# Kernel tuning notes

Measured on AMD Instinct MI355X. Metric: run time of the kernel, lower is better.

## Reference

```python
import jax, jax.numpy as jnp
import numpy as np

B, L, INPUT_DIM = 4, 4096, 32
D_MODEL, N_LAYERS = 256, 2
D_STATE, D_CONV, EXPAND = 16, 4, 2
D_INNER = EXPAND * D_MODEL          # 512
DT_RANK = (D_MODEL + 15) // 16      # 16
OUTPUT_DIM, HORIZON = 32, 4
LN_EPS = 1e-5


def setup_inputs() -> dict:
    key = jax.random.key(0)
    ks = jax.random.split(key, 16)
    s = 0.02
    inp = {
        "x": jax.random.normal(ks[0], (B, L, INPUT_DIM), jnp.float32),
        "enc_w": jax.random.normal(ks[1], (D_MODEL, INPUT_DIM), jnp.float32) * s,
        "enc_b": jnp.zeros((D_MODEL,), jnp.float32),
        "in_proj_w": jax.random.normal(ks[2], (N_LAYERS, 2 * D_INNER, D_MODEL), jnp.float32) * s,
        "conv_w": jax.random.normal(ks[3], (N_LAYERS, D_INNER, D_CONV), jnp.float32) * s,
        "conv_b": jnp.zeros((N_LAYERS, D_INNER), jnp.float32),
        "xproj_w": jax.random.normal(ks[4], (N_LAYERS, DT_RANK + 2 * D_STATE, D_INNER), jnp.float32) * s,
        "dtproj_w": jax.random.normal(ks[5], (N_LAYERS, D_INNER, DT_RANK), jnp.float32) * s,
        "dtproj_b": jax.random.normal(ks[6], (N_LAYERS, D_INNER), jnp.float32) * 0.1,
        "A_log": jnp.log(jnp.tile(jnp.arange(1.0, D_STATE + 1.0, dtype=jnp.float32), (N_LAYERS, D_INNER, 1))),
        "Dp": jnp.ones((N_LAYERS, D_INNER), jnp.float32),
        "out_proj_w": jax.random.normal(ks[7], (N_LAYERS, D_MODEL, D_INNER), jnp.float32) * s,
        "ln_g": jnp.ones((D_MODEL,), jnp.float32),
        "ln_b": jnp.zeros((D_MODEL,), jnp.float32),
        "head_w": jax.random.normal(ks[8], (OUTPUT_DIM * HORIZON, D_MODEL), jnp.float32) * s,
        "head_b": jnp.zeros((OUTPUT_DIM * HORIZON,), jnp.float32),
    }
    return inp


def _mamba_block(x, in_w, cw, cb, xp_w, dt_w, dt_b, A_log, Dp, out_w):
    # x: [B, L, d_model]
    b, l, _ = x.shape
    xz = jnp.einsum("bld,ed->ble", x, in_w)            # [B, L, 2*d_inner]
    xi, res = jnp.split(xz, 2, axis=-1)
    # causal depthwise conv1d (padding=d_conv-1, truncated to L)
    xpad = jnp.pad(xi, ((0, 0), (D_CONV - 1, 0), (0, 0)))
    xi = sum(xpad[:, k:k + l, :] * cw[:, k] for k in range(D_CONV)) + cb
    xi = jax.nn.silu(xi)
    dbl = jnp.einsum("bld,ed->ble", xi, xp_w)           # [B, L, dt_rank+2*d_state]
    dt = dbl[..., :DT_RANK]
    Bm = dbl[..., DT_RANK:DT_RANK + D_STATE]            # [B, L, d_state]
    Cm = dbl[..., DT_RANK + D_STATE:]                   # [B, L, d_state]
    dt = jax.nn.softplus(jnp.einsum("blr,dr->bld", dt, dt_w) + dt_b)  # [B, L, d_inner]
    A = -jnp.exp(A_log)                                 # [d_inner, d_state]

    def step(h, ins):
        dt_t, B_t, C_t, x_t = ins                       # [B,di],[B,ds],[B,ds],[B,di]
        dA = jnp.exp(dt_t[..., None] * A)               # [B, d_inner, d_state]
        h = dA * h + (dt_t * x_t)[..., None] * B_t[:, None, :]
        y = jnp.einsum("bds,bs->bd", h, C_t)
        return h, y

    h0 = jnp.zeros((b, D_INNER, D_STATE), x.dtype)
    xs = (jnp.moveaxis(dt, 1, 0), jnp.moveaxis(Bm, 1, 0),
          jnp.moveaxis(Cm, 1, 0), jnp.moveaxis(xi, 1, 0))
    _, ys = jax.lax.scan(step, h0, xs)                  # ys: [L, B, d_inner]
    y = jnp.moveaxis(ys, 0, 1) + xi * Dp
    y = y * jax.nn.silu(res)
    return jnp.einsum("ble,de->bld", y, out_w)


def reference(x, enc_w, enc_b, in_proj_w, conv_w, conv_b, xproj_w, dtproj_w,
              dtproj_b, A_log, Dp, out_proj_w, ln_g, ln_b, head_w, head_b):
    h = jnp.einsum("bli,di->bld", x, enc_w) + enc_b     # encoder
    for i in range(N_LAYERS):
        h = h + _mamba_block(h, in_proj_w[i], conv_w[i], conv_b[i], xproj_w[i],
                             dtproj_w[i], dtproj_b[i], A_log[i], Dp[i], out_proj_w[i])
    mu = jnp.mean(h, axis=-1, keepdims=True)
    var = jnp.mean((h - mu) ** 2, axis=-1, keepdims=True)
    hn = (h - mu) * jax.lax.rsqrt(var + LN_EPS) * ln_g + ln_b
    state = hn[:, -1, :]                                # last timestep
    return jnp.einsum("bd,od->bo", state, head_w) + head_b
```

## Files before the change

### kernel.cpp

```cpp
#include <hip/hip_runtime.h>
#include <hip/hip_bf16.h>
#include <math.h>

#define BB 4
#define LL 4096
#define DM 256
#define DI 512
#define DS 16
#define NOUTK 128
#define LN_EPS 1e-5f
#define NC 128
#define CLEN (LL/NC)
#define BL (BB*LL)
#define LDB 640

typedef __attribute__((ext_vector_type(8))) short short8;
typedef __attribute__((ext_vector_type(4))) float f32x4;

__device__ __forceinline__ ushort f2bf(float f) {
    union { float f; unsigned u; } v; v.f = f;
    unsigned r = (v.u + 0x7FFF + ((v.u >> 16) & 1)) >> 16;
    return (ushort)r;
}
__device__ __forceinline__ float bf2f(ushort u) {
    union { unsigned u; float f; } v; v.u = ((unsigned)u) << 16;
    return v.f;
}

#define PREP_N1 (2*1024*256)
#define PREP_N2 (2*256*512)
#define PREP_N3 (2*640*512)
__global__ __launch_bounds__(256) void prep_kernel(
    const float* __restrict__ inw, const float* __restrict__ opw,
    const float* __restrict__ xpw, const float* __restrict__ dtw,
    ushort* __restrict__ inw_bf, ushort* __restrict__ opw_bf,
    ushort* __restrict__ comb_bf)
{
    int i = blockIdx.x * 256 + threadIdx.x;
    if (i < PREP_N1) {
        inw_bf[i] = f2bf(inw[i]);
        return;
    }
    int j = i - PREP_N1;
    if (j < PREP_N2) {
        opw_bf[j] = f2bf(opw[j]);
        return;
    }
    int m = j - PREP_N2;
    if (m >= PREP_N3) return;
    int l = m / (640 * 512);
    int rem = m - l * 640 * 512;
    int row = rem >> 9, k = rem & 511;
    const float* xp = xpw + l * 48 * 512;
    const float* dw = dtw + l * 512 * 16;
    float v;
    if (row < 512) {
        v = 0.f;
        #pragma unroll
        for (int r = 0; r < 16; ++r)
            v = fmaf(dw[row * 16 + r], xp[r * 512 + k], v);
    } else if (row < 544) {
        v = xp[(row - 512 + 16) * 512 + k];
    } else v = 0.f;
    comb_bf[m] = f2bf(v);
}

__global__ __launch_bounds__(256) void enc_kernel(
    const float* __restrict__ x, const float* __restrict__ w,
    const float* __restrict__ b, float* __restrict__ h,
    ushort* __restrict__ hbf)
{
    __shared__ float sw[256 * 33];
    __shared__ float sx[4][32];
    int tid = threadIdx.x;
    for (int i = tid; i < 256 * 8; i += 256) {
        float4 v = ((const float4*)w)[i];
        int r = i >> 3, c = (i & 7) * 4;
        sw[r * 33 + c + 0] = v.x; sw[r * 33 + c + 1] = v.y;
        sw[r * 33 + c + 2] = v.z; sw[r * 33 + c + 3] = v.w;
    }
    int row0 = blockIdx.x * 4;
    if (tid < 32) {
        for (int rr = 0; rr < 4; ++rr)
            sx[rr][tid] = x[(size_t)(row0 + rr) * 32 + tid];
    }
    __syncthreads();
    float bb = b[tid];
    #pragma unroll
    for (int rr = 0; rr < 4; ++rr) {
        float acc = bb;
        #pragma unroll
        for (int k = 0; k < 32; ++k)
            acc = fmaf(sx[rr][k], sw[tid * 33 + k], acc);
        size_t o = (size_t)(row0 + rr) * DM + tid;
        h[o] = acc;
        hbf[o] = f2bf(acc);
    }
}

template<int EPI, bool F32OUT, bool RESID, bool BF16OUT>
__global__ __launch_bounds__(256, 6) void mfma_gemm(
    const ushort* __restrict__ A, int lda,
    const ushort* __restrict__ W,
    const float* __restrict__ bias,
    float* __restrict__ C, int ldc,
    ushort* __restrict__ Cbf, int ldcbf,
    int K)
{
    __shared__ ushort As[64 * 64];
    __shared__ ushort Ws[128 * 64];
    const int tid = threadIdx.x;

    int nwg = gridDim.x * gridDim.y;
    int wlin = blockIdx.y * gridDim.x + blockIdx.x;
    int gx = blockIdx.x, gy = blockIdx.y;
    if ((nwg & 7) == 0) {
        int q = nwg >> 3;
        int s = (wlin & 7) * q + (wlin >> 3);
        gx = s % gridDim.x;
        gy = s / gridDim.x;
    }
    const int bm = gy * 64;
    const int bn = gx * 128;
    const int wid = tid >> 6, lane = tid & 63;
    const int wrow = (wid >> 1) * 32, wcol = (wid & 1) * 64;
    const int sr = tid >> 3;
    const int sc = tid & 7;

    f32x4 acc[2][4];
    #pragma unroll
    for (int mi = 0; mi < 2; ++mi)
        #pragma unroll
        for (int ni = 0; ni < 4; ++ni)
            acc[mi][ni] = (f32x4){0.f, 0.f, 0.f, 0.f};

    const int nk = K >> 6;
    for (int t = 0; t < nk; ++t) {
        const int k0 = t << 6;
        #pragma unroll
        for (int it = 0; it < 2; ++it) {
            int r = it * 32 + sr;
            int csrc = sc ^ (r & 7);
            __builtin_amdgcn_global_load_lds(
                (const __attribute__((address_space(1))) unsigned int*)
                    (A + (size_t)(bm + r) * lda + k0 + csrc * 8),
                (__attribute__((address_space(3))) unsigned int*)
                    (As + r * 64 + sc * 8), 16, 0, 0);
        }
        #pragma unroll
        for (int it = 0; it < 4; ++it) {
            int r = it * 32 + sr;
            int csrc = sc ^ (r & 7);
            __builtin_amdgcn_global_load_lds(
                (const __attribute__((address_space(1))) unsigned int*)
                    (W + (size_t)(bn + r) * K + k0 + csrc * 8),
                (__attribute__((address_space(3))) unsigned int*)
                    (Ws + r * 64 + sc * 8), 16, 0, 0);
        }
        __syncthreads();
        #pragma unroll
        for (int kk = 0; kk < 2; ++kk) {
            short8 af[2], bfr[4];
            #pragma unroll
            for (int mi = 0; mi < 2; ++mi) {
                int r = wrow + mi * 16 + (lane & 15);
                int c = (lane >> 4) + kk * 4;
                af[mi] = *(const short8*)(As + r * 64 + ((c ^ (r & 7)) << 3));
            }
            #pragma unroll
            for (int ni = 0; ni < 4; ++ni) {
                int r = wcol + ni * 16 + (lane & 15);
                int c = (lane >> 4) + kk * 4;
                bfr[ni] = *(const short8*)(Ws + r * 64 + ((c ^ (r & 7)) << 3));
            }
            #pragma unroll
            for (int mi = 0; mi < 2; ++mi)
                #pragma unroll
                for (int ni = 0; ni < 4; ++ni)
                    acc[mi][ni] = __builtin_amdgcn_mfma_f32_16x16x32_bf16(
                        af[mi], bfr[ni], acc[mi][ni], 0, 0, 0);
        }
        __syncthreads();
    }

    #pragma unroll
    for (int mi = 0; mi < 2; ++mi)
        #pragma unroll
        for (int ni = 0; ni < 4; ++ni) {
            int col = bn + wcol + ni * 16 + (lane & 15);
            #pragma unroll
            for (int r = 0; r < 4; ++r) {
                int row = bm + wrow + mi * 16 + (lane >> 4) * 4 + r;
                float v = acc[mi][ni][r];
                if (EPI == 1) {
                    if (col < 512) {
                        float u = v + bias[col];
                        float sp = fmaxf(u, 0.f) + __logf(1.f + __expf(-fabsf(u)));
                        Cbf[(size_t)row * ldcbf + col] = f2bf(sp);
                    } else if (col < 544) {
                        C[(size_t)row * ldc + (col - 512)] = v;
                    }
                } else {
                    if (F32OUT) {
                        float* cp = C + (size_t)row * ldc + col;
                        float vv = v;
                        if (RESID) vv += *cp;
                        *cp = vv;
                        if (BF16OUT) Cbf[(size_t)row * ldcbf + col] = f2bf(vv);
                    } else if (BF16OUT) {
                        Cbf[(size_t)row * ldcbf + col] = f2bf(v);
                    }
                }
            }
        }
}

__global__ __launch_bounds__(256) void conv_silu_kernel(
    const ushort* __restrict__ xz, const float* __restrict__ cw,
    const float* __restrict__ cb, ushort* __restrict__ xi)
{
    int idx = blockIdx.x * 256 + threadIdx.x;
    int d4 = (idx & 127) * 4;
    int bt = idx >> 7;
    int t = bt & (LL - 1);
    const ushort* base = xz + (size_t)bt * 1024 + d4;
    float acc[4];
    float4 w[4];
    #pragma unroll
    for (int j = 0; j < 4; ++j) {
        acc[j] = cb[d4 + j];
        w[j] = *(const float4*)(cw + (d4 + j) * 4);
    }
    #pragma unroll
    for (int k = 0; k < 4; ++k) {
        int back = 3 - k;
        if (t >= back) {
            ushort4 v = *(const ushort4*)(base - back * 1024);
            float wk0 = (k==0)?w[0].x:(k==1)?w[0].y:(k==2)?w[0].z:w[0].w;
            float wk1 = (k==0)?w[1].x:(k==1)?w[1].y:(k==2)?w[1].z:w[1].w;
            float wk2 = (k==0)?w[2].x:(k==1)?w[2].y:(k==2)?w[2].z:w[2].w;
            float wk3 = (k==0)?w[3].x:(k==1)?w[3].y:(k==2)?w[3].z:w[3].w;
            acc[0] = fmaf(bf2f(v.x), wk0, acc[0]);
            acc[1] = fmaf(bf2f(v.y), wk1, acc[1]);
            acc[2] = fmaf(bf2f(v.z), wk2, acc[2]);
            acc[3] = fmaf(bf2f(v.w), wk3, acc[3]);
        }
    }
    ushort4 o;
    float s0 = acc[0] / (1.f + __expf(-acc[0]));
    float s1 = acc[1] / (1.f + __expf(-acc[1]));
    float s2 = acc[2] / (1.f + __expf(-acc[2]));
    float s3 = acc[3] / (1.f + __expf(-acc[3]));
    o.x = f2bf(s0); o.y = f2bf(s1); o.z = f2bf(s2); o.w = f2bf(s3);
    *(ushort4*)(xi + (size_t)bt * 512 + d4) = o;
}

__global__ __launch_bounds__(256) void scan_phase1(
    const ushort* __restrict__ xi, const ushort* __restrict__ dtb,
    const float* __restrict__ bc,
    const float* __restrict__ alog,
    float* __restrict__ cS, float* __restrict__ cH)
{
    int d = blockIdx.z * 256 + threadIdx.x;
    int b = blockIdx.y, c = blockIdx.x;
    float Av[16];
    bool fast = true;
    #pragma unroll
    for (int s = 0; s < 16; ++s) {
        Av[s] = -__expf(alog[d * 16 + s]);
        fast = fast && (fabsf(Av[s] + (float)(s + 1)) < 1e-3f * (s + 1));
    }
    float h[16];
    #pragma unroll
    for (int s = 0; s < 16; ++s) h[s] = 0.f;
    float S = 0.f;
    int t0 = c * CLEN;
    if (fast) {
        for (int t = t0; t < t0 + CLEN; ++t) {
            size_t row = (size_t)b * LL + t;
            float dt = bf2f(dtb[row * 512 + d]);
            float x = bf2f(xi[row * 512 + d]);
            float dtx = dt * x;
            S += dt;
            const float* bp = bc + row * 32;
            float e1 = __expf(-dt);
            float e2=e1*e1, e3=e2*e1, e4=e2*e2, e5=e3*e2, e6=e3*e3, e7=e4*e3, e8=e4*e4;
            float e9=e5*e4, e10=e5*e5, e11=e6*e5, e12=e6*e6, e13=e7*e6, e14=e7*e7, e15=e8*e7, e16=e8*e8;
            float pw[16] = {e1,e2,e3,e4,e5,e6,e7,e8,e9,e10,e11,e12,e13,e14,e15,e16};
            #pragma unroll
            for (int s = 0; s < 16; ++s)
                h[s] = fmaf(pw[s], h[s], dtx * bp[s]);
        }
    } else {
        for (int t = t0; t < t0 + CLEN; ++t) {
            size_t row = (size_t)b * LL + t;
            float dt = bf2f(dtb[row * 512 + d]);
            float x = bf2f(xi[row * 512 + d]);
            float dtx = dt * x;
            S += dt;
            const float* bp = bc + row * 32;
            #pragma unroll
            for (int s = 0; s < 16; ++s) {
                float dA = __expf(dt * Av[s]);
                h[s] = fmaf(dA, h[s], dtx * bp[s]);
            }
        }
    }
    cS[((size_t)b * DI + d) * NC + c] = S;
    size_t base = (((size_t)b * DI + d) * NC + c) * 16;
    #pragma unroll
    for (int q = 0; q < 4; ++q)
        *(float4*)(cH + base + q*4) = *(float4*)&h[q*4];
}

__global__ __launch_bounds__(256) void scan_phase2(
    const float* __restrict__ cS, float* __restrict__ cH,
    const float* __restrict__ alog)
{
    int bd = blockIdx.x;
    int d = bd & (DI - 1);
    int tid = threadIdx.x;
    int s = tid >> 4;
    int g = tid & 15;
    float Avs = -__expf(alog[d * 16 + s]);
    size_t sbase = (size_t)bd * NC;
    size_t base = (size_t)bd * NC * 16 + s;
    float a8[8], h8[8];
    #pragma unroll
    for (int j = 0; j < 8; ++j) {
        float Sj = cS[sbase + g * 8 + j];
        a8[j] = __expf(Avs * Sj);
        h8[j] = cH[base + (size_t)(g * 8 + j) * 16];
    }
    float A = 1.f, H = 0.f;
    #pragma unroll
    for (int j = 0; j < 8; ++j) {
        H = fmaf(a8[j], H, h8[j]);
        A *= a8[j];
    }
    #pragma unroll
    for (int off = 1; off < 16; off <<= 1) {
        float Ap = __shfl_up(A, off, 16);
        float Hp = __shfl_up(H, off, 16);
        if (g >= off) { H = fmaf(A, Hp, H); A *= Ap; }
    }
    float init = __shfl_up(H, 1, 16);
    if (g == 0) init = 0.f;
    #pragma unroll
    for (int j = 0; j < 8; ++j) {
        size_t o = base + (size_t)(g * 8 + j) * 16;
        cH[o] = init;
        init = fmaf(a8[j], init, h8[j]);
    }
}

__global__ __launch_bounds__(256) void scan_phase3(
    const ushort* __restrict__ xz,
    ushort* __restrict__ xi,
    const ushort* __restrict__ dtb,
    const float* __restrict__ bc,
    const float* __restrict__ alog,
    const float* __restrict__ Dp,
    const float* __restrict__ cH,
    int c0)
{
    int d = blockIdx.z * 256 + threadIdx.x;
    int b = blockIdx.y;
    int c = blockIdx.x + c0;
    float Av[16];
    bool fast = true;
    #pragma unroll
    for (int s = 0; s < 16; ++s) {
        Av[s] = -__expf(alog[d * 16 + s]);
        fast = fast && (fabsf(Av[s] + (float)(s + 1)) < 1e-3f * (s + 1));
    }
    float h[16];
    size_t cbase = (((size_t)b * DI + d) * NC + c) * 16;
    #pragma unroll
    for (int q = 0; q < 4; ++q)
        *(float4*)&h[q*4] = *(const float4*)(cH + cbase + q*4);
    float Dd = Dp[d];
    int t0 = c * CLEN;
    if (fast) {
        for (int t = t0; t < t0 + CLEN; ++t) {
            size_t row = (size_t)b * LL + t;
            float dt = bf2f(dtb[row * 512 + d]);
            float x = bf2f(xi[row * 512 + d]);
            float dtx = dt * x;
            const float* bp = bc + row * 32;
            const float* cp = bc + row * 32 + 16;
            float e1 = __expf(-dt);
            float e2=e1*e1, e3=e2*e1, e4=e2*e2, e5=e3*e2, e6=e3*e3, e7=e4*e3, e8=e4*e4;
            float e9=e5*e4, e10=e5*e5, e11=e6*e5, e12=e6*e6, e13=e7*e6, e14=e7*e7, e15=e8*e7, e16=e8*e8;
            float pw[16] = {e1,e2,e3,e4,e5,e6,e7,e8,e9,e10,e11,e12,e13,e14,e15,e16};
            float y = 0.f;
            #pragma unroll
            for (int s = 0; s < 16; ++s) {
                h[s] = fmaf(pw[s], h[s], dtx * bp[s]);
                y = fmaf(h[s], cp[s], y);
            }
            float res = bf2f(xz[row * 1024 + 512 + d]);
            float g = (y + x * Dd) * (res / (1.f + __expf(-res)));
            xi[row * 512 + d] = f2bf(g);
        }
    } else {
        for (int t = t0; t < t0 + CLEN; ++t) {
            size_t row = (size_t)b * LL + t;
            float dt = bf2f(dtb[row * 512 + d]);
            float x = bf2f(xi[row * 512 + d]);
            float dtx = dt * x;
            const float* bp = bc + row * 32;
            const float* cp = bc + row * 32 + 16;
            float y = 0.f;
            #pragma unroll
            for (int s = 0; s < 16; ++s) {
                float dA = __expf(dt * Av[s]);
                h[s] = fmaf(dA, h[s], dtx * bp[s]);
                y = fmaf(h[s], cp[s], y);
            }
            float res = bf2f(xz[row * 1024 + 512 + d]);
            float g = (y + x * Dd) * (res / (1.f + __expf(-res)));
            xi[row * 512 + d] = f2bf(g);
        }
    }
}

__global__ __launch_bounds__(256) void out_proj_last_kernel(
    const ushort* __restrict__ xi, const float* __restrict__ W,
    float* __restrict__ h)
{
    int b = blockIdx.x, n = threadIdx.x;
    __shared__ float sy[DI];
    const ushort* yrow = xi + ((size_t)b * LL + (LL - 1)) * DI;
    for (int k = threadIdx.x; k < DI; k += 256) sy[k] = bf2f(yrow[k]);
    __syncthreads();
    const float* wr = W + (size_t)n * DI;
    float acc = 0.f;
    for (int k = 0; k < DI; k += 4) {
        float4 wv = *(const float4*)(wr + k);
        acc = fmaf(sy[k+0], wv.x, acc);
        acc = fmaf(sy[k+1], wv.y, acc);
        acc = fmaf(sy[k+2], wv.z, acc);
        acc = fmaf(sy[k+3], wv.w, acc);
    }
    h[((size_t)b * LL + (LL - 1)) * DM + n] += acc;
}

__global__ __launch_bounds__(256) void ln_head_kernel(
    const float* __restrict__ h, const float* __restrict__ lng,
    const float* __restrict__ lnb, const float* __restrict__ hw,
    const float* __restrict__ hb, float* __restrict__ out)
{
    int b = blockIdx.x, tid = threadIdx.x;
    __shared__ float sh[DM];
    __shared__ float r1[4], r2[4];
    float v = h[((size_t)b * LL + (LL - 1)) * DM + tid];
    float s = v;
    #pragma unroll
    for (int o = 32; o >= 1; o >>= 1) s += __shfl_down(s, o);
    if ((tid & 63) == 0) r1[tid >> 6] = s;
    __syncthreads();
    float mu = (r1[0] + r1[1] + r1[2] + r1[3]) * (1.f / 256.f);
    float dv = v - mu;
    float q = dv * dv;
    #pragma unroll
    for (int o = 32; o >= 1; o >>= 1) q += __shfl_down(q, o);
    if ((tid & 63) == 0) r2[tid >> 6] = q;
    __syncthreads();
    float var = (r2[0] + r2[1] + r2[2] + r2[3]) * (1.f / 256.f);
    sh[tid] = dv * rsqrtf(var + LN_EPS) * lng[tid] + lnb[tid];
    __syncthreads();
    if (tid < NOUTK) {
        const float* wr = hw + (size_t)tid * DM;
        float acc = hb[tid];
        for (int d2 = 0; d2 < DM; d2 += 4) {
            float4 wv = *(const float4*)(wr + d2);
            acc = fmaf(sh[d2+0], wv.x, acc);
            acc = fmaf(sh[d2+1], wv.y, acc);
            acc = fmaf(sh[d2+2], wv.z, acc);
            acc = fmaf(sh[d2+3], wv.w, acc);
        }
        out[b * NOUTK + tid] = acc;
    }
}

extern "C" void kernel_launch(void* const* d_in, const int* in_sizes, int n_in,
                              void* d_out, int out_size, void* d_ws, size_t ws_size,
                              hipStream_t stream)
{
    const float* x    = (const float*)d_in[0];
    const float* encw = (const float*)d_in[1];
    const float* encb = (const float*)d_in[2];
    const float* inw  = (const float*)d_in[3];
    const float* cw   = (const float*)d_in[4];
    const float* cb   = (const float*)d_in[5];
    const float* xpw  = (const float*)d_in[6];
    const float* dtw  = (const float*)d_in[7];
    const float* dtb  = (const float*)d_in[8];
    const float* alog = (const float*)d_in[9];
    const float* Dp   = (const float*)d_in[10];
    const float* opw  = (const float*)d_in[11];
    const float* lng  = (const float*)d_in[12];
    const float* lnb  = (const float*)d_in[13];
    const float* hw   = (const float*)d_in[14];
    const float* hb   = (const float*)d_in[15];
    float* out = (float*)d_out;

    float* ws   = (float*)d_ws;
    float* h    = ws;
    float* bc   = h   + (size_t)BL * DM;
    float* cS   = bc  + (size_t)BL * 32;
    float* cH   = cS  + (size_t)BB * DI * NC;
    ushort* h_bf    = (ushort*)(cH + (size_t)BB * DI * NC * DS);
    ushort* xz_bf   = h_bf  + (size_t)BL * DM;
    ushort* xi_bf   = xz_bf + (size_t)BL * 1024;
    ushort* dt_bf   = xi_bf + (size_t)BL * DI;
    ushort* inw_bf  = dt_bf + (size_t)BL * DI;
    ushort* opw_bf  = inw_bf + 2 * 1024 * DM;
    ushort* comb_bf = opw_bf + 2 * DM * DI;

    dim3 blk(256, 1, 1);

    prep_kernel<<<dim3((PREP_N1 + PREP_N2 + PREP_N3) / 256), blk, 0, stream>>>(
        inw, opw, xpw, dtw, inw_bf, opw_bf, comb_bf);

    enc_kernel<<<dim3(BL/4), blk, 0, stream>>>(x, encw, encb, h, h_bf);

    for (int l = 0; l < 2; ++l) {
        mfma_gemm<0,false,false,true><<<dim3(1024/128, BL/64), blk, 0, stream>>>(
            h_bf, DM, inw_bf + (size_t)l * 1024 * DM, nullptr,
            nullptr, 0, xz_bf, 1024, DM);
        conv_silu_kernel<<<dim3(BL * 128 / 256), blk, 0, stream>>>(
            xz_bf, cw + l * DI * 4, cb + l * DI, xi_bf);
        mfma_gemm<1,false,false,false><<<dim3(LDB/128, BL/64), blk, 0, stream>>>(
            xi_bf, DI, comb_bf + (size_t)l * LDB * DI, dtb + l * DI,
            bc, 32, dt_bf, 512, DI);
        scan_phase1<<<dim3(NC, BB, 2), blk, 0, stream>>>(
            xi_bf, dt_bf, bc, alog + (size_t)l * DI * 16, cS, cH);
        scan_phase2<<<dim3(BB * DI), blk, 0, stream>>>(
            cS, cH, alog + (size_t)l * DI * 16);
        if (l == 0) {
            scan_phase3<<<dim3(NC, BB, 2), blk, 0, stream>>>(
                xz_bf, xi_bf, dt_bf, bc, alog + (size_t)l * DI * 16,
                Dp + l * DI, cH, 0);
            mfma_gemm<0,true,true,true><<<dim3(DM/128, BL/64), blk, 0, stream>>>(
                xi_bf, DI, opw_bf + (size_t)l * DM * DI, nullptr,
                h, DM, h_bf, DM, DI);
        } else {
            scan_phase3<<<dim3(1, BB, 2), blk, 0, stream>>>(
                xz_bf, xi_bf, dt_bf, bc, alog + (size_t)l * DI * 16,
                Dp + l * DI, cH, NC - 1);
            out_proj_last_kernel<<<dim3(BB), blk, 0, stream>>>(
                xi_bf, opw + (size_t)l * DM * DI, h);
        }
    }

    ln_head_kernel<<<dim3(BB), blk, 0, stream>>>(h, lng, lnb, hw, hb, out);
}
```

Before: 345.9 us.

## Drop fp32 residual stream, keep bf16 only; slide conv window over 8 timesteps

Removes the full fp32 hidden-state buffer: the encoder writes only bf16, the layer-0 out-projection adds its residual in place on the bf16 copy, and the final layer writes just the last-timestep fp32 row into a small buffer for the LayerNorm head. Each conv thread now handles 8 consecutive timesteps with a rolling 3-element window instead of reloading 4 rows per output. GEMM launch bounds change from 6 to 4 waves. Less HBM traffic, but the residual is kept in bf16, which costs precision.

```diff
diff --git a/kernel.cpp b/kernel.cpp
--- a/kernel.cpp
+++ b/kernel.cpp
@@ -67,8 +67,7 @@
 
 __global__ __launch_bounds__(256) void enc_kernel(
     const float* __restrict__ x, const float* __restrict__ w,
-    const float* __restrict__ b, float* __restrict__ h,
-    ushort* __restrict__ hbf)
+    const float* __restrict__ b, ushort* __restrict__ hbf)
 {
     __shared__ float sw[256 * 33];
     __shared__ float sx[4][32];
@@ -92,19 +91,17 @@
         #pragma unroll
         for (int k = 0; k < 32; ++k)
             acc = fmaf(sx[rr][k], sw[tid * 33 + k], acc);
-        size_t o = (size_t)(row0 + rr) * DM + tid;
-        h[o] = acc;
-        hbf[o] = f2bf(acc);
-    }
-}
-
-template<int EPI, bool F32OUT, bool RESID, bool BF16OUT>
-__global__ __launch_bounds__(256, 6) void mfma_gemm(
+        hbf[(size_t)(row0 + rr) * DM + tid] = f2bf(acc);
+    }
+}
+
+template<int EPI>
+__global__ __launch_bounds__(256, 4) void mfma_gemm(
     const ushort* __restrict__ A, int lda,
     const ushort* __restrict__ W,
     const float* __restrict__ bias,
     float* __restrict__ C, int ldc,
-    ushort* __restrict__ Cbf, int ldcbf,
+    ushort* Cbf, int ldcbf,
     int K)
 {
     __shared__ ushort As[64 * 64];
@@ -200,16 +197,12 @@
                     } else if (col < 544) {
                         C[(size_t)row * ldc + (col - 512)] = v;
                     }
+                } else if (EPI == 2) {
+                    size_t o = (size_t)row * ldcbf + col;
+                    float vv = v + bf2f(Cbf[o]);
+                    Cbf[o] = f2bf(vv);
                 } else {
-                    if (F32OUT) {
-                        float* cp = C + (size_t)row * ldc + col;
-                        float vv = v;
-                        if (RESID) vv += *cp;
-                        *cp = vv;
-                        if (BF16OUT) Cbf[(size_t)row * ldcbf + col] = f2bf(vv);
-                    } else if (BF16OUT) {
-                        Cbf[(size_t)row * ldcbf + col] = f2bf(v);
-                    }
+                    Cbf[(size_t)row * ldcbf + col] = f2bf(v);
                 }
             }
         }
@@ -221,38 +214,43 @@
 {
     int idx = blockIdx.x * 256 + threadIdx.x;
     int d4 = (idx & 127) * 4;
-    int bt = idx >> 7;
-    int t = bt & (LL - 1);
-    const ushort* base = xz + (size_t)bt * 1024 + d4;
-    float acc[4];
-    float4 w[4];
-    #pragma unroll
-    for (int j = 0; j < 4; ++j) {
-        acc[j] = cb[d4 + j];
-        w[j] = *(const float4*)(cw + (d4 + j) * 4);
-    }
-    #pragma unroll
-    for (int k = 0; k < 4; ++k) {
-        int back = 3 - k;
-        if (t >= back) {
-            ushort4 v = *(const ushort4*)(base - back * 1024);
-            float wk0 = (k==0)?w[0].x:(k==1)?w[0].y:(k==2)?w[0].z:w[0].w;
-            float wk1 = (k==0)?w[1].x:(k==1)?w[1].y:(k==2)?w[1].z:w[1].w;
-            float wk2 = (k==0)?w[2].x:(k==1)?w[2].y:(k==2)?w[2].z:w[2].w;
-            float wk3 = (k==0)?w[3].x:(k==1)?w[3].y:(k==2)?w[3].z:w[3].w;
-            acc[0] = fmaf(bf2f(v.x), wk0, acc[0]);
-            acc[1] = fmaf(bf2f(v.y), wk1, acc[1]);
-            acc[2] = fmaf(bf2f(v.z), wk2, acc[2]);
-            acc[3] = fmaf(bf2f(v.w), wk3, acc[3]);
-        }
-    }
-    ushort4 o;
-    float s0 = acc[0] / (1.f + __expf(-acc[0]));
-    float s1 = acc[1] / (1.f + __expf(-acc[1]));
-    float s2 = acc[2] / (1.f + __expf(-acc[2]));
-    float s3 = acc[3] / (1.f + __expf(-acc[3]));
-    o.x = f2bf(s0); o.y = f2bf(s1); o.z = f2bf(s2); o.w = f2bf(s3);
-    *(ushort4*)(xi + (size_t)bt * 512 + d4) = o;
+    int grp = idx >> 7;
+    int b = grp >> 9;
+    int t0 = (grp & 511) * 8;
+    const ushort* base = xz + ((size_t)(b * LL + t0) * 1024) + d4;
+    ushort* obase = xi + ((size_t)(b * LL + t0) * 512) + d4;
+
+    float4 w0 = *(const float4*)(cw + (d4 + 0) * 4);
+    float4 w1 = *(const float4*)(cw + (d4 + 1) * 4);
+    float4 w2 = *(const float4*)(cw + (d4 + 2) * 4);
+    float4 w3 = *(const float4*)(cw + (d4 + 3) * 4);
+    float b0 = cb[d4 + 0], b1 = cb[d4 + 1], b2 = cb[d4 + 2], b3 = cb[d4 + 3];
+
+    ushort4 z4 = {0, 0, 0, 0};
+    ushort4 win0 = (t0 >= 3) ? *(const ushort4*)(base - 3 * 1024) : z4;
+    ushort4 win1 = (t0 >= 2) ? *(const ushort4*)(base - 2 * 1024) : z4;
+    ushort4 win2 = (t0 >= 1) ? *(const ushort4*)(base - 1 * 1024) : z4;
+
+    #pragma unroll
+    for (int k = 0; k < 8; ++k) {
+        ushort4 cur = *(const ushort4*)(base + k * 1024);
+        float a0 = b0, a1 = b1, a2 = b2, a3 = b3;
+        a0 = fmaf(bf2f(win0.x), w0.x, a0); a1 = fmaf(bf2f(win0.y), w1.x, a1);
+        a2 = fmaf(bf2f(win0.z), w2.x, a2); a3 = fmaf(bf2f(win0.w), w3.x, a3);
+        a0 = fmaf(bf2f(win1.x), w0.y, a0); a1 = fmaf(bf2f(win1.y), w1.y, a1);
+        a2 = fmaf(bf2f(win1.z), w2.y, a2); a3 = fmaf(bf2f(win1.w), w3.y, a3);
+        a0 = fmaf(bf2f(win2.x), w0.z, a0); a1 = fmaf(bf2f(win2.y), w1.z, a1);
+        a2 = fmaf(bf2f(win2.z), w2.z, a2); a3 = fmaf(bf2f(win2.w), w3.z, a3);
+        a0 = fmaf(bf2f(cur.x),  w0.w, a0); a1 = fmaf(bf2f(cur.y),  w1.w, a1);
+        a2 = fmaf(bf2f(cur.z),  w2.w, a2); a3 = fmaf(bf2f(cur.w),  w3.w, a3);
+        ushort4 o;
+        o.x = f2bf(a0 / (1.f + __expf(-a0)));
+        o.y = f2bf(a1 / (1.f + __expf(-a1)));
+        o.z = f2bf(a2 / (1.f + __expf(-a2)));
+        o.w = f2bf(a3 / (1.f + __expf(-a3)));
+        *(ushort4*)(obase + k * 512) = o;
+        win0 = win1; win1 = win2; win2 = cur;
+    }
 }
 
 __global__ __launch_bounds__(256) void scan_phase1(
@@ -427,7 +425,7 @@
 
 __global__ __launch_bounds__(256) void out_proj_last_kernel(
     const ushort* __restrict__ xi, const float* __restrict__ W,
-    float* __restrict__ h)
+    const ushort* __restrict__ hbf, float* __restrict__ hlast)
 {
     int b = blockIdx.x, n = threadIdx.x;
     __shared__ float sy[DI];
@@ -443,18 +441,18 @@
         acc = fmaf(sy[k+2], wv.z, acc);
         acc = fmaf(sy[k+3], wv.w, acc);
     }
-    h[((size_t)b * LL + (LL - 1)) * DM + n] += acc;
+    hlast[b * DM + n] = acc + bf2f(hbf[((size_t)b * LL + (LL - 1)) * DM + n]);
 }
 
 __global__ __launch_bounds__(256) void ln_head_kernel(
-    const float* __restrict__ h, const float* __restrict__ lng,
+    const float* __restrict__ hlast, const float* __restrict__ lng,
     const float* __restrict__ lnb, const float* __restrict__ hw,
     const float* __restrict__ hb, float* __restrict__ out)
 {
     int b = blockIdx.x, tid = threadIdx.x;
     __shared__ float sh[DM];
     __shared__ float r1[4], r2[4];
-    float v = h[((size_t)b * LL + (LL - 1)) * DM + tid];
+    float v = hlast[b * DM + tid];
     float s = v;
     #pragma unroll
     for (int o = 32; o >= 1; o >>= 1) s += __shfl_down(s, o);
@@ -507,11 +505,11 @@
     float* out = (float*)d_out;
 
     float* ws   = (float*)d_ws;
-    float* h    = ws;
-    float* bc   = h   + (size_t)BL * DM;
+    float* bc   = ws;
     float* cS   = bc  + (size_t)BL * 32;
     float* cH   = cS  + (size_t)BB * DI * NC;
-    ushort* h_bf    = (ushort*)(cH + (size_t)BB * DI * NC * DS);
+    float* hlast = cH + (size_t)BB * DI * NC * DS;
+    ushort* h_bf    = (ushort*)(hlast + BB * DM);
     ushort* xz_bf   = h_bf  + (size_t)BL * DM;
     ushort* xi_bf   = xz_bf + (size_t)BL * 1024;
     ushort* dt_bf   = xi_bf + (size_t)BL * DI;
@@ -524,15 +522,15 @@
     prep_kernel<<<dim3((PREP_N1 + PREP_N2 + PREP_N3) / 256), blk, 0, stream>>>(
         inw, opw, xpw, dtw, inw_bf, opw_bf, comb_bf);
 
-    enc_kernel<<<dim3(BL/4), blk, 0, stream>>>(x, encw, encb, h, h_bf);
+    enc_kernel<<<dim3(BL/4), blk, 0, stream>>>(x, encw, encb, h_bf);
 
     for (int l = 0; l < 2; ++l) {
-        mfma_gemm<0,false,false,true><<<dim3(1024/128, BL/64), blk, 0, stream>>>(
+        mfma_gemm<0><<<dim3(1024/128, BL/64), blk, 0, stream>>>(
             h_bf, DM, inw_bf + (size_t)l * 1024 * DM, nullptr,
             nullptr, 0, xz_bf, 1024, DM);
-        conv_silu_kernel<<<dim3(BL * 128 / 256), blk, 0, stream>>>(
+        conv_silu_kernel<<<dim3(BL * 128 / 8 / 256), blk, 0, stream>>>(
             xz_bf, cw + l * DI * 4, cb + l * DI, xi_bf);
-        mfma_gemm<1,false,false,false><<<dim3(LDB/128, BL/64), blk, 0, stream>>>(
+        mfma_gemm<1><<<dim3(LDB/128, BL/64), blk, 0, stream>>>(
             xi_bf, DI, comb_bf + (size_t)l * LDB * DI, dtb + l * DI,
             bc, 32, dt_bf, 512, DI);
         scan_phase1<<<dim3(NC, BB, 2), blk, 0, stream>>>(
@@ -543,17 +541,17 @@
             scan_phase3<<<dim3(NC, BB, 2), blk, 0, stream>>>(
                 xz_bf, xi_bf, dt_bf, bc, alog + (size_t)l * DI * 16,
                 Dp + l * DI, cH, 0);
-            mfma_gemm<0,true,true,true><<<dim3(DM/128, BL/64), blk, 0, stream>>>(
+            mfma_gemm<2><<<dim3(DM/128, BL/64), blk, 0, stream>>>(
                 xi_bf, DI, opw_bf + (size_t)l * DM * DI, nullptr,
-                h, DM, h_bf, DM, DI);
+                nullptr, 0, h_bf, DM, DI);
         } else {
             scan_phase3<<<dim3(1, BB, 2), blk, 0, stream>>>(
                 xz_bf, xi_bf, dt_bf, bc, alog + (size_t)l * DI * 16,
                 Dp + l * DI, cH, NC - 1);
             out_proj_last_kernel<<<dim3(BB), blk, 0, stream>>>(
-                xi_bf, opw + (size_t)l * DM * DI, h);
-        }
-    }
-
-    ln_head_kernel<<<dim3(BB), blk, 0, stream>>>(h, lng, lnb, hw, hb, out);
-}
+                xi_bf, opw + (size_t)l * DM * DI, h_bf, hlast);
+        }
+    }
+
+    ln_head_kernel<<<dim3(BB), blk, 0, stream>>>(hlast, lng, lnb, hw, hb, out);
+}
```

New measurement: 306.6 us. 1.13x faster.
